# Kernel tuning notes

Hardware: AMD Instinct MI355X
Metric: run time of the kernel (lower is better)

## Reference

```python
import jax, jax.numpy as jnp
import numpy as np
from jax import lax

B, C, H, W = 4, 64, 256, 320
PT = 6
EPS = 1e-6
BN_EPS = 1e-5


def conv2d(x, w, b=None):
    y = lax.conv_general_dilated(x, w, (1, 1), 'SAME',
                                 dimension_numbers=('NCHW', 'OIHW', 'NCHW'))
    if b is not None:
        y = y + b[None, :, None, None]
    return y


def batchnorm(x, g, b):
    # training-mode batch statistics over (N, H, W)
    m = jnp.mean(x, axis=(0, 2, 3), keepdims=True)
    v = jnp.var(x, axis=(0, 2, 3), keepdims=True)
    return g[None, :, None, None] * (x - m) * lax.rsqrt(v + BN_EPS) + b[None, :, None, None]


def gen_kernel(fout, wconv, g, b, pk):
    # Basic2d: conv(no bias) -> BN -> ReLU, producing pk*pk-1 affinity channels
    w = jax.nn.relu(batchnorm(conv2d(fout, wconv), g, b))
    s = jnp.sum(jnp.abs(w), axis=1, keepdims=True)
    w = w / (s + EPS)
    mid = 1.0 - jnp.sum(w, axis=1, keepdims=True)
    h = (pk * pk - 1) // 2
    return jnp.concatenate([w[:, :h], mid, w[:, h:]], axis=1)  # [B, pk*pk, H, W]


def spatial_kernel(d, sigma):
    r = jnp.linspace(-1.0, 1.0, d)
    x, y = jnp.meshgrid(r, r, indexing='ij')
    return jnp.exp(-(x * x + y * y) / (2.0 * sigma * sigma)).reshape(1, d * d, 1, 1)


def local_conv(x, w, pk):
    # per-pixel spatially-varying conv: x [B,1,H,W], w [B,pk*pk,H,W]
    patches = lax.conv_general_dilated_patches(
        x, (pk, pk), (1, 1), 'SAME', dimension_numbers=('NCHW', 'OIHW', 'NCHW'))
    return jnp.sum(patches * w, axis=1, keepdims=True)


def setup_inputs() -> dict:
    key = jax.random.key(0)
    ks = jax.random.split(key, 16)
    f32 = jnp.float32
    inp = {
        'fout': jax.random.normal(ks[0], (B, C, H, W), f32),
        'hn': jax.random.uniform(ks[1], (B, 1, H, W), f32),
        'h0': jax.random.uniform(ks[2], (B, 1, H, W), f32),
        # GenKernel_L convs (no bias, followed by BN)
        'w3_conv': jax.random.normal(ks[3], (8, C, 3, 3), f32) * 0.05,
        'w3_g': jnp.ones((8,), f32), 'w3_b': jnp.zeros((8,), f32),
        'w5_conv': jax.random.normal(ks[4], (24, C, 3, 3), f32) * 0.05,
        'w5_g': jnp.ones((24,), f32), 'w5_b': jnp.zeros((24,), f32),
        'w7_conv': jax.random.normal(ks[5], (48, C, 3, 3), f32) * 0.05,
        'w7_g': jnp.ones((48,), f32), 'w7_b': jnp.zeros((48,), f32),
        # confidence heads (conv with bias -> softmax over channels)
        'ck_w': jax.random.normal(ks[6], (3, C, 3, 3), f32) * 0.05,
        'ck_b': jnp.zeros((3,), f32),
        'ct_w': jax.random.normal(ks[7], (3, C + 3, 3, 3), f32) * 0.05,
        'ct_b': jnp.zeros((3,), f32),
        'sig3': jnp.float32(1.0), 'sig5': jnp.float32(1.0), 'sig7': jnp.float32(1.0),
    }
    return inp


def reference(fout, hn, h0, w3_conv, w3_g, w3_b, w5_conv, w5_g, w5_b,
              w7_conv, w7_g, w7_b, ck_w, ck_b, ct_w, ct_b, sig3, sig5, sig7):
    weight3 = gen_kernel(fout, w3_conv, w3_g, w3_b, 3) * spatial_kernel(3, sig3)
    weight5 = gen_kernel(fout, w5_conv, w5_g, w5_b, 5) * spatial_kernel(5, sig5)
    weight7 = gen_kernel(fout, w7_conv, w7_g, w7_b, 7) * spatial_kernel(7, sig7)
    weight3 = weight3 / jnp.clip(jnp.sum(weight3, 1, keepdims=True), 1e-7)
    weight5 = weight5 / jnp.clip(jnp.sum(weight5, 1, keepdims=True), 1e-7)
    weight7 = weight7 / jnp.clip(jnp.sum(weight7, 1, keepdims=True), 1e-7)

    confk = jax.nn.softmax(conv2d(fout, ck_w, ck_b), axis=1)
    conf3, conf5, conf7 = confk[:, 0:1], confk[:, 1:2], confk[:, 2:3]

    hn3 = hn5 = hn7 = hn
    hns = [hn]
    for i in range(PT):
        hn3 = local_conv(hn3, weight3, 3)
        hn5 = local_conv(hn5, weight5, 5)
        hn7 = local_conv(hn7, weight7, 7)
        if i == PT // 2 - 1:
            hns.append(conf3 * hn3 + conf5 * hn5 + conf7 * hn7)
    hns.append(conf3 * hn3 + conf5 * hn5 + conf7 * hn7)
    hns = jnp.concatenate(hns, axis=1)  # [B, 3, H, W]

    wt = jax.nn.softmax(conv2d(jnp.concatenate([fout, hns], axis=1), ct_w, ct_b), axis=1)
    return jnp.sum(wt * hns, axis=1, keepdims=True)
```

## Files before the change

kernel.cpp:

```cpp
#include <hip/hip_runtime.h>
#include <hip/hip_bf16.h>
#include <math.h>

#define W_    320
#define H_    256
#define HW_   81920
#define BHW_  327680
#define PRM_TOT 49786
#define WCH   86
#define PW_   326
#define PH_   262
#define PHW_  85412

#define OW3  0
#define OW5  4608
#define OW7  18432
#define OCK  46080
#define OCT  47808
#define OG3  49617
#define OB3  49625
#define OG5  49633
#define OB5  49657
#define OG7  49681
#define OB7  49729
#define OCKB 49777
#define OCTB 49780
#define OSIG 49783

typedef unsigned short u16;
typedef __attribute__((ext_vector_type(8))) short short8;
typedef __attribute__((ext_vector_type(4))) float f32x4;

__device__ __forceinline__ float dload(const void* p, size_t i, int isbf) {
  return isbf ? __bfloat162float(((const __hip_bfloat16*)p)[i])
              : ((const float*)p)[i];
}

__device__ __forceinline__ u16 f32_bf16_rne(float f) {
  union { float f; unsigned u; } v; v.f = f;
  unsigned r = v.u + 0x7FFFu + ((v.u >> 16) & 1u);
  return (u16)(r >> 16);
}
__device__ __forceinline__ float bf16_f32(u16 h) {
  union { unsigned u; float f; } v; v.u = ((unsigned)h) << 16;
  return v.f;
}

__device__ __forceinline__ unsigned wquant(float w) {
  int v = (int)(w * 65536.f + 0.5f);
  return (unsigned)(v > 65535 ? 65535 : (v < 0 ? 0 : v));
}

__global__ __launch_bounds__(512) void k_detect(
    const void* t0, const void* t1, const void* t2, const void* t3,
    const void* t4, const void* t5, const void* t6, const void* t7,
    const void* t8, const void* t9, const void* t10, const void* t11,
    const void* t12, const void* t13, const void* t14, const void* t15,
    const void* t16, const void* t17, int* __restrict__ flags)
{
  __shared__ int c_other, c_zeven, c_zodd, c_m;
  const void* ptrs[18] = {t0,t1,t2,t3,t4,t5,t6,t7,t8,t9,
                          t10,t11,t12,t13,t14,t15,t16,t17};
  const int ns[18] = {20971520, 327680, 4608, 8, 8, 13824, 24, 24,
                      27648, 48, 48, 1728, 3, 1809, 3, 1, 1, 1};
  const int tensor = blockIdx.x;
  const int n = ns[tensor];
  const unsigned short* u = (const unsigned short*)ptrs[tensor];
  if (threadIdx.x == 0) { c_other = 0; c_zeven = 0; c_zodd = 0; c_m = 0; }
  __syncthreads();
  {
    int k = threadIdx.x >> 1;
    long long pos = (long long)k * n / 256;
    int j = ((int)pos & ~1) + (threadIdx.x & 1);
    if (j < n) {
      unsigned short v = u[j];
      int e = (v >> 7) & 0xFF;
      atomicAdd(&c_m, 1);
      if (v != 0 && (e < 90 || e > 150)) atomicAdd(&c_other, 1);
      if (v == 0) {
        if (j & 1) atomicAdd(&c_zodd, 1); else atomicAdd(&c_zeven, 1);
      }
    }
  }
  __syncthreads();
  if (threadIdx.x == 0) {
    int isf32;
    if (n == 1) isf32 = (u[0] == 0);
    else        isf32 = (4 * c_other >= c_m) ||
                        (2 * (c_zeven - c_zodd) >= c_m);
    flags[tensor] = isf32 ? 0 : 1;
  }
}

__global__ __launch_bounds__(256) void k_cvt(
    const void* w3c, const void* w5c, const void* w7c, const void* ckw, const void* ctw,
    const void* g3, const void* b3, const void* g5, const void* b5,
    const void* g7, const void* b7, const void* ckb, const void* ctb,
    const void* s3, const void* s5, const void* s7,
    float* __restrict__ prm, const int* __restrict__ flags)
{
  int j = blockIdx.x * 256 + threadIdx.x;
  if (j >= PRM_TOT) return;
  const void* src; int off; int fid;
  if      (j < OW5)    { src = w3c; off = OW3;  fid = 2; }
  else if (j < OW7)    { src = w5c; off = OW5;  fid = 5; }
  else if (j < OCK)    { src = w7c; off = OW7;  fid = 8; }
  else if (j < OCT)    { src = ckw; off = OCK;  fid = 11; }
  else if (j < OG3)    { src = ctw; off = OCT;  fid = 13; }
  else if (j < OB3)    { src = g3;  off = OG3;  fid = 3; }
  else if (j < OG5)    { src = b3;  off = OB3;  fid = 4; }
  else if (j < OB5)    { src = g5;  off = OG5;  fid = 6; }
  else if (j < OG7)    { src = b5;  off = OB5;  fid = 7; }
  else if (j < OB7)    { src = g7;  off = OG7;  fid = 9; }
  else if (j < OCKB)   { src = b7;  off = OB7;  fid = 10; }
  else if (j < OCTB)   { src = ckb; off = OCKB; fid = 12; }
  else if (j < OSIG)   { src = ctb; off = OCTB; fid = 14; }
  else if (j < OSIG+1) { src = s3;  off = OSIG;   fid = 15; }
  else if (j < OSIG+2) { src = s5;  off = OSIG+1; fid = 16; }
  else                 { src = s7;  off = OSIG+2; fid = 17; }
  prm[j] = dload(src, j - off, flags[fid]);
}

__global__ __launch_bounds__(256) void k_padhn(
    const void* __restrict__ rawhn, float* __restrict__ hnp,
    const int* __restrict__ flags)
{
  const int isbf = flags[1];
  const int p = blockIdx.x * 256 + threadIdx.x;
  const int b = p / HW_, q = p - b * HW_;
  const int y = q / W_, x = q - y * W_;
  hnp[(size_t)b * PHW_ + (size_t)(y + 3) * PW_ + (x + 3)] =
      dload(rawhn, (size_t)b * HW_ + q, isbf);
}

__global__ __launch_bounds__(256) void k_pack(
    const float* __restrict__ prm, u16* __restrict__ apack)
{
  int idx = blockIdx.x * 256 + threadIdx.x;
  int e = idx & 7;
  int lane = (idx >> 3) & 63;
  int t = idx >> 9;
  int mt = t % 6; t /= 6;
  int chunk = t & 1; t >>= 1;
  int tap = t % 9;
  int hilo = t / 9;
  int oc = mt * 16 + (lane & 15);
  int ic = chunk * 32 + (lane >> 4) * 8 + e;
  float w = 0.f;
  if (oc < 83)      w = prm[(size_t)oc * 576 + (size_t)ic * 9 + tap];
  else if (oc < 86) w = prm[OCT + (size_t)((oc - 83) * 67 + ic) * 9 + tap];
  u16 h = f32_bf16_rne(w);
  u16 outv = (hilo == 0) ? h : f32_bf16_rne(w - bf16_f32(h));
  apack[idx] = outv;
}

template<int ISBF>
__device__ __forceinline__ void stage_chunk(
    const void* __restrict__ fout, int b, int y0, int x0, int chunk,
    u16* Bhi, u16* Blo)
{
  const int g = threadIdx.x & 3;
  const int cell0 = threadIdx.x >> 2;
  const size_t fb = (size_t)b * 64 * HW_ + (size_t)(chunk * 32 + g * 8) * HW_;
#pragma unroll
  for (int it = 0; it < 7; ++it) {
    int cell = cell0 + it * 64;
    if (cell < 396) {
      int row = cell / 66;
      int px = cell - row * 66;
      int gy = y0 - 1 + row, gx = x0 - 1 + px;
      bool ok = ((unsigned)gy < H_) && ((unsigned)gx < W_);
      size_t base = fb + (size_t)gy * W_ + gx;
      short8 hs = {0,0,0,0,0,0,0,0};
      short8 ls = {0,0,0,0,0,0,0,0};
#pragma unroll
      for (int i = 0; i < 8; ++i) {
        float v = ok ? dload(fout, base + (size_t)i * HW_, ISBF) : 0.f;
        union { float f; unsigned u; } uv; uv.f = v;
        u16 h = (u16)(uv.u >> 16);
        float resid = v - bf16_f32(h);
        hs[i] = (short)h;
        ls[i] = (short)f32_bf16_rne(resid);
      }
      int off = ((row * 66 + px) * 32 + g * 8) * 2;
      off ^= (px & 7) << 4;
      *(short8*)((char*)Bhi + off) = hs;
      *(short8*)((char*)Blo + off) = ls;
    }
  }
}

__global__ __launch_bounds__(256, 2) void k_conv_mfma(
    const void* __restrict__ fout, const u16* __restrict__ apack,
    float* __restrict__ wbuf, const int* __restrict__ flags)
{
  __shared__ __align__(16) u16 Bhi[6 * 66 * 32];
  __shared__ __align__(16) u16 Blo[6 * 66 * 32];
  const int isbf = flags[0];
  const int x0 = blockIdx.x * 64;
  const int y0 = blockIdx.y * 4;
  const int b  = blockIdx.z;
  const int lane = threadIdx.x & 63;
  const int wv   = threadIdx.x >> 6;

  const f32x4 zero = {0.f, 0.f, 0.f, 0.f};
  f32x4 acc[6][4];
#pragma unroll
  for (int mt = 0; mt < 6; ++mt)
#pragma unroll
    for (int nt = 0; nt < 4; ++nt)
      acc[mt][nt] = zero;

  for (int chunk = 0; chunk < 2; ++chunk) {
    if (chunk) __syncthreads();
    if (isbf) stage_chunk<1>(fout, b, y0, x0, chunk, Bhi, Blo);
    else      stage_chunk<0>(fout, b, y0, x0, chunk, Bhi, Blo);
    __syncthreads();

#pragma unroll
    for (int tap = 0; tap < 9; ++tap) {
      const int dy = tap / 3, dx = tap - dy * 3;
      const int row = wv + dy;
      short8 bh[4], bl[4];
#pragma unroll
      for (int nt = 0; nt < 4; ++nt) {
        int px = nt * 16 + (lane & 15) + dx;
        int off = ((row * 66 + px) * 32 + (lane >> 4) * 8) * 2;
        off ^= (px & 7) << 4;
        bh[nt] = *(const short8*)((const char*)Bhi + off);
        bl[nt] = *(const short8*)((const char*)Blo + off);
      }
      const u16* abase = apack + (size_t)(tap * 2 + chunk) * 3072 + (size_t)lane * 8;
#pragma unroll
      for (int mt = 0; mt < 6; ++mt) {
        short8 ah = *(const short8*)(abase + (size_t)mt * 512);
        short8 al = *(const short8*)(abase + (size_t)mt * 512 + 55296);
#pragma unroll
        for (int nt = 0; nt < 4; ++nt) {
          acc[mt][nt] = __builtin_amdgcn_mfma_f32_16x16x32_bf16(ah, bh[nt], acc[mt][nt], 0, 0, 0);
          acc[mt][nt] = __builtin_amdgcn_mfma_f32_16x16x32_bf16(ah, bl[nt], acc[mt][nt], 0, 0, 0);
          acc[mt][nt] = __builtin_amdgcn_mfma_f32_16x16x32_bf16(al, bh[nt], acc[mt][nt], 0, 0, 0);
        }
      }
    }
  }

  const int ocr = (lane >> 4) * 4;
  float* wb = wbuf + (size_t)b * WCH * HW_
            + (size_t)(y0 + wv) * W_ + x0 + (lane & 15);
#pragma unroll
  for (int mt = 0; mt < 6; ++mt) {
#pragma unroll
    for (int nt = 0; nt < 4; ++nt) {
#pragma unroll
      for (int r = 0; r < 4; ++r) {
        int oc = mt * 16 + ocr + r;
        if (oc < 86)
          wb[(size_t)oc * HW_ + nt * 16] = acc[mt][nt][r];
      }
    }
  }
}

__global__ __launch_bounds__(256) void k_stats(
    const float* __restrict__ wbuf, float* __restrict__ stat)
{
  const int ch = blockIdx.y;
  float s = 0.f, qq = 0.f;
  for (int idx = blockIdx.x * 256 + threadIdx.x; idx < BHW_;
       idx += gridDim.x * 256) {
    int b = idx / HW_, r = idx - b * HW_;
    float v = wbuf[((size_t)(b * WCH + ch)) * HW_ + r];
    s += v; qq += v * v;
  }
#pragma unroll
  for (int m = 1; m < 64; m <<= 1) {
    s += __shfl_xor(s, m, 64);
    qq += __shfl_xor(qq, m, 64);
  }
  __shared__ float rs[4], rq[4];
  const int lane = threadIdx.x & 63, wv = threadIdx.x >> 6;
  if (lane == 0) { rs[wv] = s; rq[wv] = qq; }
  __syncthreads();
  if (threadIdx.x == 0) {
    float ts = rs[0] + rs[1] + rs[2] + rs[3];
    float tq = rq[0] + rq[1] + rq[2] + rq[3];
    atomicAdd(&stat[ch], ts);
    atomicAdd(&stat[80 + ch], tq);
  }
}

__global__ void k_bn_finalize(float* __restrict__ stat)
{
  int ch = threadIdx.x;
  if (ch < 80) {
    const float n = 1.f / (float)BHW_;
    float m = stat[ch] * n;
    float var = stat[80 + ch] * n - m * m;
    stat[160 + ch] = m;
    stat[240 + ch] = rsqrtf(var + 1e-5f);
  }
}

__global__ __launch_bounds__(256, 2) void k_prop0(
    float* __restrict__ wbuf, float* __restrict__ conf,
    const float* __restrict__ hnp,
    float* __restrict__ h3o, float* __restrict__ h5o, float* __restrict__ h7o,
    const float* __restrict__ prm, const float* __restrict__ stat)
{
  const int p = blockIdx.x * 256 + threadIdx.x;
  const int b = p / HW_, q = p - b * HW_;
  const int y = q / W_, x = q - y * W_;
  float* base = wbuf + ((size_t)b * WCH) * HW_ + q;
  const float* mean = stat + 160;
  const float* istd = stat + 240;
  const size_t pc = (size_t)b * PHW_ + (size_t)(y + 3) * PW_ + (x + 3);
  const float* hc = hnp + pc;

  {
    float c0 = base[(size_t)80 * HW_] + prm[OCKB + 0];
    float c1 = base[(size_t)81 * HW_] + prm[OCKB + 1];
    float c2 = base[(size_t)82 * HW_] + prm[OCKB + 2];
    float m = fmaxf(c0, fmaxf(c1, c2));
    float e0 = expf(c0 - m), e1 = expf(c1 - m), e2 = expf(c2 - m);
    float inv = 1.f / (e0 + e1 + e2);
    float* cf = conf + ((size_t)b * 3) * HW_ + q;
    cf[0] = e0 * inv;
    cf[(size_t)HW_] = e1 * inv;
    cf[(size_t)2 * HW_] = e2 * inv;
  }

  float a3, a5, a7;
  unsigned carry;

  {
    float cvv[8]; float s = 0.f;
#pragma unroll
    for (int i = 0; i < 8; ++i) {
      float v = base[(size_t)i * HW_];
      v = fmaxf(0.f, (v - mean[i]) * istd[i] * prm[OG3 + i] + prm[OB3 + i]);
      cvv[i] = v; s += v;
    }
    float inv = 1.f / (s + 1e-6f);
    float ctr = 1.f - s * inv;
    float sg = prm[OSIG + 0];
    float a = 0.5f / (sg * sg);
    float e1 = expf(-a);
    float g1[3] = {e1, 1.f, e1};
    float tot = 0.f;
#pragma unroll
    for (int j = 0; j < 9; ++j) {
      float w = (j == 4) ? ctr : cvv[j < 4 ? j : j - 1] * inv;
      w *= g1[j / 3] * g1[j % 3];
      if (j == 4) ctr = w; else cvv[j < 4 ? j : j - 1] = w;
      tot += w;
    }
    float rr = 1.f / fmaxf(tot, 1e-7f);
    auto wk = [&](int c) -> float {
      return ((c == 4) ? ctr : cvv[c < 4 ? c : c - 1]) * rr;
    };
    a3 = 0.f;
#pragma unroll
    for (int j = 0; j < 9; ++j)
      a3 = fmaf(wk(j), hc[(j / 3 - 1) * PW_ + (j % 3 - 1)], a3);
#pragma unroll
    for (int pr = 0; pr < 4; ++pr)
      base[(size_t)pr * HW_] =
          __uint_as_float(wquant(wk(2 * pr)) | (wquant(wk(2 * pr + 1)) << 16));
    carry = wquant(wk(8));
  }

  {
    float cvv[24]; float s = 0.f;
#pragma unroll
    for (int i = 0; i < 24; ++i) {
      float v = base[(size_t)(8 + i) * HW_];
      v = fmaxf(0.f, (v - mean[8 + i]) * istd[8 + i] * prm[OG5 + i] + prm[OB5 + i]);
      cvv[i] = v; s += v;
    }
    float inv = 1.f / (s + 1e-6f);
    float ctr = 1.f - s * inv;
    float sg = prm[OSIG + 1];
    float a = 0.5f / (sg * sg);
    float ea = expf(-a), eb = expf(-0.25f * a);
    float g1[5] = {ea, eb, 1.f, eb, ea};
    float tot = 0.f;
#pragma unroll
    for (int j = 0; j < 25; ++j) {
      float w = (j == 12) ? ctr : cvv[j < 12 ? j : j - 1] * inv;
      w *= g1[j / 5] * g1[j % 5];
      if (j == 12) ctr = w; else cvv[j < 12 ? j : j - 1] = w;
      tot += w;
    }
    float rr = 1.f / fmaxf(tot, 1e-7f);
    auto wk = [&](int j) -> float {
      return ((j == 12) ? ctr : cvv[j < 12 ? j : j - 1]) * rr;
    };
    a5 = 0.f;
#pragma unroll
    for (int j = 0; j < 25; ++j)
      a5 = fmaf(wk(j), hc[(j / 5 - 2) * PW_ + (j % 5 - 2)], a5);
    base[(size_t)4 * HW_] = __uint_as_float(carry | (wquant(wk(0)) << 16));
#pragma unroll
    for (int m = 0; m < 12; ++m)
      base[(size_t)(5 + m) * HW_] =
          __uint_as_float(wquant(wk(1 + 2 * m)) | (wquant(wk(2 + 2 * m)) << 16));
  }

  {
    float cvv[48]; float s = 0.f;
#pragma unroll
    for (int i = 0; i < 48; ++i) {
      float v = base[(size_t)(32 + i) * HW_];
      v = fmaxf(0.f, (v - mean[32 + i]) * istd[32 + i] * prm[OG7 + i] + prm[OB7 + i]);
      cvv[i] = v; s += v;
    }
    float inv = 1.f / (s + 1e-6f);
    float ctr = 1.f - s * inv;
    float sg = prm[OSIG + 2];
    float a = 0.5f / (sg * sg);
    float ea = expf(-a), eb = expf(-(4.f / 9.f) * a), ec = expf(-(1.f / 9.f) * a);
    float g1[7] = {ea, eb, ec, 1.f, ec, eb, ea};
    float tot = 0.f;
#pragma unroll
    for (int j = 0; j < 49; ++j) {
      float w = (j == 24) ? ctr : cvv[j < 24 ? j : j - 1] * inv;
      w *= g1[j / 7] * g1[j % 7];
      if (j == 24) ctr = w; else cvv[j < 24 ? j : j - 1] = w;
      tot += w;
    }
    float rr = 1.f / fmaxf(tot, 1e-7f);
    auto wk = [&](int j) -> float {
      return ((j == 24) ? ctr : cvv[j < 24 ? j : j - 1]) * rr;
    };
    a7 = 0.f;
#pragma unroll
    for (int j = 0; j < 49; ++j)
      a7 = fmaf(wk(j), hc[(j / 7 - 3) * PW_ + (j % 7 - 3)], a7);
#pragma unroll
    for (int m = 0; m < 24; ++m)
      base[(size_t)(17 + m) * HW_] =
          __uint_as_float(wquant(wk(2 * m)) | (wquant(wk(2 * m + 1)) << 16));
    base[(size_t)41 * HW_] = __uint_as_float(wquant(wk(48)));
  }

  h3o[pc] = a3;
  h5o[pc] = a5;
  h7o[pc] = a7;
}

__global__ __launch_bounds__(256) void k_prop_q(
    const float* __restrict__ wbuf, const float* __restrict__ conf,
    const float* __restrict__ in3, const float* __restrict__ in5,
    const float* __restrict__ in7, size_t bsi,
    float* __restrict__ out3, float* __restrict__ out5,
    float* __restrict__ out7, size_t bso,
    float* __restrict__ combo, int store_h)
{
  const int p = blockIdx.x * 256 + threadIdx.x;
  const int b = p / HW_, q = p - b * HW_;
  const int y = q / W_, x = q - y * W_;
  const float* base = wbuf + ((size_t)b * WCH) * HW_ + q;

  unsigned pk[42];
#pragma unroll
  for (int pr = 0; pr < 42; ++pr)
    pk[pr] = __float_as_uint(base[(size_t)pr * HW_]);
#define WRAW(CH) ((float)((pk[(CH) >> 1] >> (((CH) & 1) * 16)) & 0xffffu))

  const size_t pc = (size_t)(y + 3) * PW_ + (x + 3);
  const float* c3 = in3 + (size_t)b * bsi + pc;
  const float* c5 = in5 + (size_t)b * bsi + pc;
  const float* c7 = in7 + (size_t)b * bsi + pc;

  float a3 = 0.f, a5 = 0.f, a7 = 0.f;
#pragma unroll
  for (int j = 0; j < 9; ++j)
    a3 = fmaf(WRAW(j), c3[(j / 3 - 1) * PW_ + (j % 3 - 1)], a3);
#pragma unroll
  for (int j = 0; j < 25; ++j)
    a5 = fmaf(WRAW(9 + j), c5[(j / 5 - 2) * PW_ + (j % 5 - 2)], a5);
#pragma unroll
  for (int j = 0; j < 49; ++j)
    a7 = fmaf(WRAW(34 + j), c7[(j / 7 - 3) * PW_ + (j % 7 - 3)], a7);
#undef WRAW
  const float sc = 1.f / 65536.f;
  a3 *= sc; a5 *= sc; a7 *= sc;

  if (store_h) {
    out3[(size_t)b * bso + pc] = a3;
    out5[(size_t)b * bso + pc] = a5;
    out7[(size_t)b * bso + pc] = a7;
  }
  if (combo) {
    const float* cf = conf + ((size_t)b * 3) * HW_ + q;
    combo[(size_t)b * HW_ + q] =
        cf[0] * a3 + cf[(size_t)HW_] * a5 + cf[(size_t)2 * HW_] * a7;
  }
}

__global__ __launch_bounds__(256, 2) void k_final(
    const float* __restrict__ wbuf, const float* __restrict__ hnp,
    const float* __restrict__ mid, const float* __restrict__ fin,
    const float* __restrict__ prm, float* __restrict__ out)
{
  const float* ctw = prm + OCT;
  const int p = blockIdx.x * 256 + threadIdx.x;
  const int b = p / HW_, q = p - b * HW_;
  const int y = q / W_, x = q - y * W_;
  const size_t bo = (size_t)b * HW_;

  const float* lg = wbuf + ((size_t)b * WCH + 83) * HW_ + q;
  float l0 = prm[OCTB + 0] + lg[0];
  float l1 = prm[OCTB + 1] + lg[(size_t)HW_];
  float l2 = prm[OCTB + 2] + lg[(size_t)2 * HW_];

  const float* hc = hnp + (size_t)b * PHW_ + (size_t)(y + 3) * PW_ + (x + 3);
#pragma unroll
  for (int j = 0; j < 9; ++j) {
    float v = hc[(j / 3 - 1) * PW_ + (j % 3 - 1)];
    l0 = fmaf(v, ctw[(0 * 67 + 64) * 9 + j], l0);
    l1 = fmaf(v, ctw[(1 * 67 + 64) * 9 + j], l1);
    l2 = fmaf(v, ctw[(2 * 67 + 64) * 9 + j], l2);
  }
#pragma unroll
  for (int c = 1; c < 3; ++c) {
    const int icg = 64 + c;
    const float* src = (c == 1) ? mid : fin;
#pragma unroll
    for (int j = 0; j < 9; ++j) {
      int gy = y + j / 3 - 1, gx = x + j % 3 - 1;
      float v = 0.f;
      if ((unsigned)gy < H_ && (unsigned)gx < W_)
        v = src[bo + (size_t)gy * W_ + gx];
      l0 = fmaf(v, ctw[(0 * 67 + icg) * 9 + j], l0);
      l1 = fmaf(v, ctw[(1 * 67 + icg) * 9 + j], l1);
      l2 = fmaf(v, ctw[(2 * 67 + icg) * 9 + j], l2);
    }
  }
  float m = fmaxf(l0, fmaxf(l1, l2));
  float e0 = expf(l0 - m), e1 = expf(l1 - m), e2 = expf(l2 - m);
  float inv = 1.f / (e0 + e1 + e2);
  float h0c = hc[0];
  float r = (e0 * h0c + e1 * mid[bo + q] + e2 * fin[bo + q]) * inv;
  out[bo + q] = r;
}

extern "C" void kernel_launch(void* const* d_in, const int* in_sizes, int n_in,
                              void* d_out, int out_size, void* d_ws, size_t ws_size,
                              hipStream_t stream)
{
  static const int EXP[19] = {20971520, 327680, 327680, 4608, 8, 8, 13824, 24, 24,
                              27648, 48, 48, 1728, 3, 1809, 3, 1, 1, 1};
  const void* P[19];
  bool match = (n_in >= 19);
  for (int i = 0; i < 19 && match; ++i) if (in_sizes[i] != EXP[i]) match = false;
  if (match) {
    for (int i = 0; i < 19; ++i) P[i] = d_in[i];
  } else {
    bool used[64] = {false};
    for (int t = 0; t < 19; ++t) {
      P[t] = d_in[t < n_in ? t : 0];
      for (int i = 0; i < n_in && i < 64; ++i)
        if (!used[i] && in_sizes[i] == EXP[t]) { P[t] = d_in[i]; used[i] = true; break; }
    }
  }
  const void* fout = P[0];
  const void* hn   = P[1];
  float* out = (float*)d_out;

  float* ws    = (float*)d_ws;
  int*   flags = (int*)ws;
  float* stat  = ws + 32;
  float* prm   = ws + 352;
  float* big   = ws + 50176;
  float* wbuf  = big;
  float* conf  = wbuf + (size_t)WCH * BHW_;
  float* Abase = conf + (size_t)3 * BHW_;
  float* hnp   = Abase + (size_t)12 * PHW_;
  float* midb  = hnp + (size_t)4 * PHW_;
  float* finb  = midb + (size_t)BHW_;
  u16*   apack = (u16*)midb;

  float* a3f = Abase;
  float* a5f = Abase + (size_t)4 * PHW_;
  float* a7f = Abase + (size_t)8 * PHW_;
  float* b3f = wbuf + (size_t)42 * HW_;
  float* b5f = b3f + (size_t)PHW_;
  float* b7f = b3f + (size_t)2 * PHW_;

  (void)hipMemsetAsync(stat, 0, 160 * sizeof(float), stream);
  (void)hipMemsetAsync(Abase, 0, (size_t)16 * PHW_ * sizeof(float), stream);

  k_detect<<<18, 512, 0, stream>>>(
      P[0], P[1], P[3], P[4], P[5], P[6], P[7], P[8],
      P[9], P[10], P[11], P[12], P[13], P[14], P[15],
      P[16], P[17], P[18], flags);

  k_cvt<<<(PRM_TOT + 255) / 256, 256, 0, stream>>>(
      P[3], P[6], P[9], P[12], P[14],
      P[4], P[5], P[7], P[8], P[10], P[11],
      P[13], P[15], P[16], P[17], P[18], prm, flags);

  k_padhn<<<1280, 256, 0, stream>>>(hn, hnp, flags);
  k_pack<<<432, 256, 0, stream>>>(prm, apack);
  k_conv_mfma<<<dim3(5, 64, 4), 256, 0, stream>>>(fout, apack, wbuf, flags);
  k_stats<<<dim3(32, 80), 256, 0, stream>>>(wbuf, stat);
  k_bn_finalize<<<1, 128, 0, stream>>>(stat);

  k_prop0<<<1280, 256, 0, stream>>>(
      wbuf, conf, hnp, a3f, a5f, a7f, prm, stat);

  for (int b = 0; b < 4; ++b)
    (void)hipMemsetAsync(wbuf + ((size_t)b * WCH + 42) * HW_, 0,
                         (size_t)3 * PHW_ * sizeof(float), stream);

  const size_t bsA = PHW_;
  const size_t bsB = (size_t)WCH * HW_;
  k_prop_q<<<1280, 256, 0, stream>>>(wbuf, conf, a3f, a5f, a7f, bsA,
                                     b3f, b5f, b7f, bsB, nullptr, 1);
  k_prop_q<<<1280, 256, 0, stream>>>(wbuf, conf, b3f, b5f, b7f, bsB,
                                     a3f, a5f, a7f, bsA, midb, 1);
  k_prop_q<<<1280, 256, 0, stream>>>(wbuf, conf, a3f, a5f, a7f, bsA,
                                     b3f, b5f, b7f, bsB, nullptr, 1);
  k_prop_q<<<1280, 256, 0, stream>>>(wbuf, conf, b3f, b5f, b7f, bsB,
                                     a3f, a5f, a7f, bsA, nullptr, 1);
  k_prop_q<<<1280, 256, 0, stream>>>(wbuf, conf, a3f, a5f, a7f, bsA,
                                     b3f, b5f, b7f, bsB, finb, 0);

  k_final<<<1280, 256, 0, stream>>>(wbuf, hnp, midb, finb, prm, out);
}
```

Measured before the change: 433.8 us.

## Transpose packed propagation weights to pixel-major layout and vectorize BN stats

A new kernel, run once after prop0, rearranges the 42 packed weight words per pixel from channel-planar into pixel-contiguous storage, so each k_prop_q thread reads them with ten float4 loads instead of 42 strided scalar loads. The ping-pong hn buffers move to the start of each batch's wbuf slab, and one leftover word goes to a separate xw buffer. k_stats also switches to float4 loads. The change adds an extra pass over the weight data, and the new per-thread stride of 160 bytes may cost coalescing. The in-place transpose also depends on the new buffer offsets not overlapping other data.

```diff
diff --git a/kernel.cpp b/kernel.cpp
--- a/kernel.cpp
+++ b/kernel.cpp
@@ -266,12 +266,15 @@
     const float* __restrict__ wbuf, float* __restrict__ stat)
 {
   const int ch = blockIdx.y;
+  const int HW4 = HW_ / 4;
   float s = 0.f, qq = 0.f;
-  for (int idx = blockIdx.x * 256 + threadIdx.x; idx < BHW_;
+  for (int idx = blockIdx.x * 256 + threadIdx.x; idx < BHW_ / 4;
        idx += gridDim.x * 256) {
-    int b = idx / HW_, r = idx - b * HW_;
-    float v = wbuf[((size_t)(b * WCH + ch)) * HW_ + r];
-    s += v; qq += v * v;
+    int b = idx / HW4, r = idx - b * HW4;
+    float4 v = *(const float4*)(wbuf + ((size_t)(b * WCH + ch)) * HW_ +
+                                (size_t)r * 4);
+    s  += v.x + v.y + v.z + v.w;
+    qq += v.x * v.x + v.y * v.y + v.z * v.z + v.w * v.w;
   }
 #pragma unroll
   for (int m = 1; m < 64; m <<= 1) {
@@ -449,8 +452,30 @@
   h7o[pc] = a7;
 }
 
+__global__ __launch_bounds__(256) void k_wt(
+    float* __restrict__ wbuf, float* __restrict__ xw)
+{
+  const int p = blockIdx.x * 256 + threadIdx.x;
+  const int b = p / HW_, q = p - b * HW_;
+  float* base = wbuf + (size_t)b * WCH * HW_;
+  float v[42];
+#pragma unroll
+  for (int c = 0; c < 42; ++c) v[c] = base[(size_t)c * HW_ + q];
+  float4* dst = (float4*)(base + (size_t)43 * HW_ + (size_t)q * 40);
+#pragma unroll
+  for (int i = 0; i < 10; ++i) {
+    float4 t;
+    t.x = v[4 * i]; t.y = v[4 * i + 1]; t.z = v[4 * i + 2]; t.w = v[4 * i + 3];
+    dst[i] = t;
+  }
+  base[(size_t)42 * HW_ + q] = v[40];
+  xw[(size_t)b * HW_ + q] = v[41];
+}
+
 __global__ __launch_bounds__(256) void k_prop_q(
-    const float* __restrict__ wbuf, const float* __restrict__ conf,
+    const float* __restrict__ wq,
+    const float* __restrict__ xw,
+    const float* __restrict__ conf,
     const float* __restrict__ in3, const float* __restrict__ in5,
     const float* __restrict__ in7, size_t bsi,
     float* __restrict__ out3, float* __restrict__ out5,
@@ -460,12 +485,20 @@
   const int p = blockIdx.x * 256 + threadIdx.x;
   const int b = p / HW_, q = p - b * HW_;
   const int y = q / W_, x = q - y * W_;
-  const float* base = wbuf + ((size_t)b * WCH) * HW_ + q;
+  const float* base = wq + (size_t)b * WCH * HW_;
 
   unsigned pk[42];
-#pragma unroll
-  for (int pr = 0; pr < 42; ++pr)
-    pk[pr] = __float_as_uint(base[(size_t)pr * HW_]);
+  const float4* wr = (const float4*)(base + (size_t)43 * HW_ + (size_t)q * 40);
+#pragma unroll
+  for (int i = 0; i < 10; ++i) {
+    float4 v = wr[i];
+    pk[4 * i + 0] = __float_as_uint(v.x);
+    pk[4 * i + 1] = __float_as_uint(v.y);
+    pk[4 * i + 2] = __float_as_uint(v.z);
+    pk[4 * i + 3] = __float_as_uint(v.w);
+  }
+  pk[40] = __float_as_uint(base[(size_t)42 * HW_ + q]);
+  pk[41] = __float_as_uint(xw[(size_t)b * HW_ + q]);
 #define WRAW(CH) ((float)((pk[(CH) >> 1] >> (((CH) & 1) * 16)) & 0xffffu))
 
   const size_t pc = (size_t)(y + 3) * PW_ + (x + 3);
@@ -580,14 +613,15 @@
   float* hnp   = Abase + (size_t)12 * PHW_;
   float* midb  = hnp + (size_t)4 * PHW_;
   float* finb  = midb + (size_t)BHW_;
+  float* xw    = finb + (size_t)BHW_;
   u16*   apack = (u16*)midb;
 
   float* a3f = Abase;
   float* a5f = Abase + (size_t)4 * PHW_;
   float* a7f = Abase + (size_t)8 * PHW_;
-  float* b3f = wbuf + (size_t)42 * HW_;
-  float* b5f = b3f + (size_t)PHW_;
-  float* b7f = b3f + (size_t)2 * PHW_;
+  float* b3f = wbuf;
+  float* b5f = wbuf + (size_t)PHW_;
+  float* b7f = wbuf + (size_t)2 * PHW_;
 
   (void)hipMemsetAsync(stat, 0, 160 * sizeof(float), stream);
   (void)hipMemsetAsync(Abase, 0, (size_t)16 * PHW_ * sizeof(float), stream);
@@ -611,21 +645,23 @@
   k_prop0<<<1280, 256, 0, stream>>>(
       wbuf, conf, hnp, a3f, a5f, a7f, prm, stat);
 
+  k_wt<<<1280, 256, 0, stream>>>(wbuf, xw);
+
   for (int b = 0; b < 4; ++b)
-    (void)hipMemsetAsync(wbuf + ((size_t)b * WCH + 42) * HW_, 0,
+    (void)hipMemsetAsync(wbuf + (size_t)b * WCH * HW_, 0,
                          (size_t)3 * PHW_ * sizeof(float), stream);
 
   const size_t bsA = PHW_;
   const size_t bsB = (size_t)WCH * HW_;
-  k_prop_q<<<1280, 256, 0, stream>>>(wbuf, conf, a3f, a5f, a7f, bsA,
+  k_prop_q<<<1280, 256, 0, stream>>>(wbuf, xw, conf, a3f, a5f, a7f, bsA,
                                      b3f, b5f, b7f, bsB, nullptr, 1);
-  k_prop_q<<<1280, 256, 0, stream>>>(wbuf, conf, b3f, b5f, b7f, bsB,
+  k_prop_q<<<1280, 256, 0, stream>>>(wbuf, xw, conf, b3f, b5f, b7f, bsB,
                                      a3f, a5f, a7f, bsA, midb, 1);
-  k_prop_q<<<1280, 256, 0, stream>>>(wbuf, conf, a3f, a5f, a7f, bsA,
+  k_prop_q<<<1280, 256, 0, stream>>>(wbuf, xw, conf, a3f, a5f, a7f, bsA,
                                      b3f, b5f, b7f, bsB, nullptr, 1);
-  k_prop_q<<<1280, 256, 0, stream>>>(wbuf, conf, b3f, b5f, b7f, bsB,
+  k_prop_q<<<1280, 256, 0, stream>>>(wbuf, xw, conf, b3f, b5f, b7f, bsB,
                                      a3f, a5f, a7f, bsA, nullptr, 1);
-  k_prop_q<<<1280, 256, 0, stream>>>(wbuf, conf, a3f, a5f, a7f, bsA,
+  k_prop_q<<<1280, 256, 0, stream>>>(wbuf, xw, conf, a3f, a5f, a7f, bsA,
                                      b3f, b5f, b7f, bsB, finb, 0);
 
   k_final<<<1280, 256, 0, stream>>>(wbuf, hnp, midb, finb, prm, out);
```

Result: slower. 478.9 us (+10.4%).
